# Kernel tuning notes

Hardware: AMD Instinct MI355X
Metric: run time of the kernel (lower is better)

The kernel has to match this reference:

```python
import jax, jax.numpy as jnp
from jax import lax
import numpy as np

BETA, TAU, NUM_ITER = 0.33, 1.0, 5
DN = ('NCDHW', 'OIDHW', 'NCDHW')


def _base_kernels():
    # 3x3x3 neighborhood-counting kernels from the torch module
    K_N6 = np.zeros((3, 3, 3), np.float32)
    for c in [(1, 1, 0), (1, 1, 2), (1, 0, 1), (1, 2, 1), (0, 1, 1), (2, 1, 1)]:
        K_N6[c] = 1.0
    K_N26 = np.ones((3, 3, 3), np.float32); K_N26[1, 1, 1] = 0.0
    K_N18 = K_N26.copy()
    for c in [(0, 0, 0), (0, 0, 2), (0, 2, 0), (0, 2, 2), (2, 0, 0), (2, 0, 2), (2, 2, 0), (2, 2, 2)]:
        K_N18[c] = 0.0
    K_B26 = np.zeros((3, 3, 3), np.float32)
    K_B26[0, 0, 0] = 1.0
    for c in [(0, 0, 1), (0, 1, 0), (0, 1, 1), (1, 0, 0), (1, 0, 1), (1, 1, 0)]:
        K_B26[c] = -1.0
    K_A6 = np.zeros((3, 3, 3), np.float32)
    K_A6[0, 1, 1] = -1.0
    for c in [(0, 0, 1), (0, 1, 0), (0, 1, 2), (0, 2, 1)]:
        K_A6[c] = 1.0
    return K_N6, K_N26, K_N18, K_B26, K_A6


def _stacked_weight():
    # Fuse all 17 simple-check convolutions into one conv over a 3-channel input
    # channel 0: img, channel 1: 1-img, channel 2: 2*img-1
    K_N6, K_N26, K_N18, K_B26, K_A6 = _base_kernels()
    b26 = [K_B26] + [np.flip(K_B26, ax) for ax in [(0,), (1,), (2,), (0, 1), (0, 2), (1, 2), (0, 1, 2)]]
    fA = np.flip(K_A6, 0)
    a6 = [K_A6, np.rot90(K_A6, axes=(0, 1)), np.rot90(K_A6, axes=(0, 2)),
          fA, np.rot90(fA, axes=(0, 1)), np.rot90(fA, axes=(0, 2))]
    rows = []
    def put(k, ch):
        w = np.zeros((3, 3, 3, 3), np.float32)
        w[ch] = k
        rows.append(w)
    put(K_N6, 1)   # counts bg 6-neighbors (applied to 1-img)
    put(K_N26, 0)  # counts fg 26-neighbors
    put(K_N18, 0)  # counts fg 18-neighbors
    for k in b26:
        put(k, 2)  # 8 B26-cell detectors on 2*img-1
    for k in a6:
        put(k, 2)  # 6 A6-cell detectors on 2*img-1
    return jnp.asarray(np.stack(rows)), jnp.asarray(K_N26).reshape(1, 1, 3, 3, 3)


W_SIMPLE, W_N26 = _stacked_weight()


def _clip01(x):  # F.hardtanh(x, 0, 1)
    return jnp.clip(x, 0.0, 1.0)


def _endpoint_check(img):
    p = jnp.pad(img, ((0, 0), (0, 0), (1, 1), (1, 1), (1, 1)))
    n26 = lax.conv_general_dilated(p, W_N26, (1, 1, 1), 'VALID', dimension_numbers=DN)
    return _clip01(2.0 - n26)  # endpoint iff <=1 fg 26-neighbor


def _simple_check(img):
    p = jnp.pad(img, ((0, 0), (0, 0), (1, 1), (1, 1), (1, 1)))
    x3 = jnp.concatenate([p, 1.0 - p, 2.0 * p - 1.0], axis=1)
    f = lax.conv_general_dilated(x3, W_SIMPLE, (2, 2, 2), 'VALID', dimension_numbers=DN)
    n6, n26, n18 = f[:, 0:1], f[:, 1:2], f[:, 2:3]
    num_b26 = jax.nn.relu(f[:, 3:11] - 6.0).sum(axis=1, keepdims=True)
    num_a6 = jax.nn.relu(f[:, 11:17] - 4.0).sum(axis=1, keepdims=True)
    cond1 = _clip01(n6) * _clip01(2.0 - n6)                              # exactly one bg 6-neighbor
    cond2 = _clip01(n26) * _clip01(2.0 - n26)                            # exactly one fg 26-neighbor
    cond3 = _clip01(n18) * _clip01(2.0 - n18) * _clip01(1.0 - num_b26)   # one 18-neighbor, no B26 cell
    cond4 = _clip01(n6 - 1.0) * _clip01(1.0 - num_a6) * _clip01(1.0 - num_b26)  # >=2 bg 6-nb, no A6/B26 cell
    return _clip01(cond1 + cond2 + cond3 + cond4)


def _forward(img):
    # _prepare_input: zero-pad each spatial dim by 1
    img = jnp.pad(img, ((0, 0), (0, 0), (1, 1), (1, 1), (1, 1)))
    # _stochastic_discretization (reparametrization + straight-through)
    alpha = (img + 1e-8) / (1.0 - img + 1e-8)
    u = jax.random.uniform(jax.random.key(42), img.shape, img.dtype, 1e-8, 1.0 - 1e-8)
    noise = jnp.log(u) - jnp.log1p(-u)
    soft = jax.nn.sigmoid((jnp.log(alpha) + noise * BETA) / TAU)
    img = lax.stop_gradient((soft > 0.5).astype(soft.dtype) - soft) + soft
    offsets = [(0, 0, 0), (1, 0, 0), (0, 1, 0), (1, 1, 0), (0, 0, 1), (1, 0, 1), (0, 1, 1), (1, 1, 1)]
    for _ in range(NUM_ITER):
        is_end = _endpoint_check(img)
        for xo, yo, zo in offsets:
            is_simple = _simple_check(img[:, :, xo:, yo:, zo:])
            sl = (slice(None), slice(None), slice(xo, None, 2), slice(yo, None, 2), slice(zo, None, 2))
            del_cand = is_simple * (1.0 - is_end[sl])
            img = img.at[sl].set(jnp.minimum(img[sl], 1.0 - del_cand))
    # _prepare_output: strip padding
    return img[:, :, 1:-1, 1:-1, 1:-1]


def setup_inputs():
    key = jax.random.key(0)
    img = jax.random.uniform(key, (2, 1, 160, 160, 160), jnp.float32)  # probabilities in [0,1)
    return {"img": img}


def reference(img):
    return _forward(img)
```

## Files before the change

kernel.cpp:

```cpp
#include <hip/hip_runtime.h>
#include <stdint.h>

#pragma clang fp contract(off)

#define PDIM 162
#define NW   (2*PDIM*PDIM*3)
#define NWH  (NW/2)
#define OD   160

#define PZ 97
#define LADDR(lz,ly) ((lz)*PZ + (ly)*3)

__device__ __forceinline__ uint32_t rotl32(uint32_t x, uint32_t r) {
  return (x << r) | (x >> (32u - r));
}

__device__ __forceinline__ uint32_t threefry_bits(uint32_t idx) {
  const uint32_t ks0 = 0u, ks1 = 42u, ks2 = 0x1BD11BDAu ^ 0u ^ 42u;
  uint32_t x0 = 0u + ks0;
  uint32_t x1 = idx + ks1;
#define TFR(r) { x0 += x1; x1 = rotl32(x1, (r)); x1 ^= x0; }
  TFR(13u) TFR(15u) TFR(26u) TFR(6u)
  x0 += ks1; x1 += ks2 + 1u;
  TFR(17u) TFR(29u) TFR(16u) TFR(24u)
  x0 += ks2; x1 += ks0 + 2u;
  TFR(13u) TFR(15u) TFR(26u) TFR(6u)
  x0 += ks0; x1 += ks1 + 3u;
  TFR(17u) TFR(29u) TFR(16u) TFR(24u)
  x0 += ks1; x1 += ks2 + 4u;
  TFR(13u) TFR(15u) TFR(26u) TFR(6u)
  x0 += ks2; x1 += ks0 + 5u;
#undef TFR
  return x0 ^ x1;
}

__device__ __forceinline__ float xla_logf(float xin) {
  uint32_t bits = __float_as_uint(xin);
  float e = (float)((int)(bits >> 23) - 126);
  float x = __uint_as_float((bits & 0x007fffffu) | 0x3f000000u);
  const float SQRTHF = 0.707106781186547524f;
  bool lt = (x < SQRTHF);
  float tmp = lt ? x : 0.0f;
  e = e - (lt ? 1.0f : 0.0f);
  x = x - 1.0f;
  x = x + tmp;
  float z = x * x;
  float y = 7.0376836292e-2f;
  y = fmaf(y, x, -1.1514610310e-1f);
  y = fmaf(y, x,  1.1676998740e-1f);
  y = fmaf(y, x, -1.2420140846e-1f);
  y = fmaf(y, x,  1.4249322787e-1f);
  y = fmaf(y, x, -1.6668057665e-1f);
  y = fmaf(y, x,  2.0000714765e-1f);
  y = fmaf(y, x, -2.4999993993e-1f);
  y = fmaf(y, x,  3.3333331174e-1f);
  y = y * x;
  y = y * z;
  y = fmaf(e, -2.12194440e-4f, y);
  y = fmaf(-0.5f, z, y);
  x = x + y;
  x = fmaf(e, 0.693359375f, x);
  return x;
}

__device__ __forceinline__ float xla_log1pf(float x) {
  float for_large = xla_logf(x + 1.0f);
  float for_small = fmaf(-0.5f, x, 1.0f) * x;
  return (fabsf(x) < 1e-4f) ? for_small : for_large;
}

__device__ __forceinline__ bool bin_pred(const float* __restrict__ in, uint32_t w,
                                         uint32_t lane) {
  uint32_t row = w / 3u, wx = w - row * 3u;
  uint32_t n  = row / (uint32_t)(PDIM * PDIM);
  uint32_t rr = row - n * (uint32_t)(PDIM * PDIM);
  uint32_t z  = rr / (uint32_t)PDIM;
  uint32_t y  = rr - z * (uint32_t)PDIM;
  uint32_t x  = wx * 64u + lane;
  if ((z - 1u) >= 160u || (y - 1u) >= 160u || (x - 1u) >= 160u) return false;
  float v = in[((n * 160u + (z - 1u)) * 160u + (y - 1u)) * 160u + (x - 1u)];
  uint32_t i = row * 162u + x;
  uint32_t b = threefry_bits(i);
  float f  = __uint_as_float((b >> 9) | 0x3f800000u) - 1.0f;
  float uu = fmaxf(1e-8f, f + 1e-8f);
  float la = xla_logf((v + 1e-8f) / ((1.0f - v) + 1e-8f));
  float noise = xla_logf(uu) - xla_log1pf(-uu);
  float zs = la + noise * 0.33f;
  return (zs > 1.1920928955078125e-7f);
}

__global__ __launch_bounds__(256) void k_binarize(const float* __restrict__ in,
                                                  uint64_t* __restrict__ bits) {
  uint32_t t = blockIdx.x * 256u + threadIdx.x;
  uint32_t w0 = t >> 6, lane = t & 63u;
  if (w0 >= (uint32_t)NWH) return;
  uint32_t w1 = w0 + (uint32_t)NWH;
  bool p0 = bin_pred(in, w0, lane);
  bool p1 = bin_pred(in, w1, lane);
  uint64_t m0 = __ballot(p0);
  uint64_t m1 = __ballot(p1);
  if (lane == 0) { bits[w0] = m0; bits[w1] = m1; }
}

#define NB(dz,dy,dx) ((dx)==-1 ? Lb[(dz)+1][(dy)+1] : ((dx)==1 ? Rb[(dz)+1][(dy)+1] : Vv[(dz)+1][(dy)+1]))

#define GATHER_W(SRC, lz, ly, w) \
  _Pragma("unroll") \
  for (int dz = 0; dz < 3; ++dz) \
    _Pragma("unroll") \
    for (int dy = 0; dy < 3; ++dy) { \
      int rb = LADDR((lz) + dz - 1, (ly) + dy - 1); \
      uint64_t r0 = SRC[rb], r1 = SRC[rb + 1], r2 = SRC[rb + 2]; \
      uint64_t b = ((w) == 0) ? r0 : (((w) == 1) ? r1 : r2); \
      uint64_t a = ((w) == 0) ? 0ull : (((w) == 1) ? r0 : r1); \
      uint64_t d = ((w) == 0) ? r1 : (((w) == 1) ? r2 : 0ull); \
      Vv[dz][dy] = b; \
      Lb[dz][dy] = (b << 1) | (a >> 63); \
      Rb[dz][dy] = (b >> 1) | (d << 63); \
    }

__global__ __launch_bounds__(1024) void k_iter(const uint64_t* __restrict__ bin,
                                               uint64_t* __restrict__ bout,
                                               float4* __restrict__ outf,
                                               int zero_pads) {
  __shared__ uint64_t Bt[32 * PZ];
  __shared__ uint64_t Ge[32 * PZ];
  const int tid = threadIdx.x;
  const int bid = blockIdx.x;
  const int n  = bid / 100;
  const int rm = bid - n * 100;
  const int tz = rm / 10, ty = rm - tz * 10;
  const int gz0 = 1 + 16 * tz, gy0 = 1 + 16 * ty;

  if (zero_pads && bid == 0) {
    for (int j = tid; j < 1288; j += 1024) {
      int nn, z, y;
      if (j < 648) { nn = j / 324; int r = j - nn * 324;
                     z = (r >= 162) ? 161 : 0; y = (r >= 162) ? r - 162 : r; }
      else { int j2 = j - 648; nn = j2 / 320; int r = j2 - nn * 320;
             y = (r >= 160) ? 161 : 0; z = 1 + ((r >= 160) ? r - 160 : r); }
      uint64_t* p = bout + (((nn * 162 + z) * 162) + y) * 3;
      p[0] = 0; p[1] = 0; p[2] = 0;
    }
  }

  for (int ti = tid; ti < 32 * 32 * 3; ti += 1024) {
    int w = ti % 3, r = ti / 3, ly = r % 32, lz = r / 32;
    int z = gz0 - 8 + lz, y = gy0 - 8 + ly;
    uint64_t v = 0;
    if ((unsigned)z < 162u && (unsigned)y < 162u)
      v = bin[((n * 162 + z) * 162 + y) * 3 + w];
    Bt[LADDR(lz, ly) + w] = v;
  }
  __syncthreads();

  for (int ti = tid; ti < 30 * 30 * 3; ti += 1024) {
    int w = ti % 3, r = ti / 3, iy = r % 30, iz = r / 30;
    int lz = 1 + iz, ly = 1 + iy;
    int base = LADDR(lz, ly) + w;
    uint64_t res = 0;
    if (Bt[base] != 0ull) {
      uint64_t Vv[3][3], Lb[3][3], Rb[3][3];
      GATHER_W(Bt, lz, ly, w)
      uint64_t s = 0, c = 0;
#define ACC(bb) { uint64_t _b = (bb); c |= s & _b; s |= _b; }
#pragma unroll
      for (int dz = -1; dz <= 1; ++dz)
#pragma unroll
        for (int dy = -1; dy <= 1; ++dy) {
          ACC(NB(dz,dy,-1)); ACC(NB(dz,dy,1));
          if (dz != 0 || dy != 0) ACC(NB(dz,dy,0));
        }
#undef ACC
      res = c;
    }
    Ge[base] = res;
  }
  __syncthreads();

  const int PLZ[8] = {1,0,1,0,1,0,1,0};
  const int PLY[8] = {1,1,0,0,1,1,0,0};
  for (int k = 0; k < 8; ++k) {
    const int h = 7 - k, cnt1 = 8 + h;
    const uint64_t xmask = (k < 4) ? 0x5555555555555555ull : 0xAAAAAAAAAAAAAAAAull;
    int s0 = 8 - h;
    const int slz = s0 + ((s0 ^ PLZ[k]) & 1);
    const int sly = s0 + ((s0 ^ PLY[k]) & 1);
    for (int ti = tid; ti < cnt1 * cnt1 * 3; ti += 1024) {
      int w = ti % 3, r = ti / 3, iy = r % cnt1, iz = r / cnt1;
      int lz = slz + 2 * iz, ly = sly + 2 * iy;
      int base = LADDR(lz, ly) + w;
      uint64_t center = Bt[base];
      uint64_t active = center & xmask & Ge[base];
      if (active == 0ull) continue;
      uint64_t Vv[3][3], Lb[3][3], Rb[3][3];
      GATHER_W(Bt, lz, ly, w)

      uint64_t on = 0, tw = 0, fo = 0;
#define C6ADD(b) { uint64_t _u = on & (b); on ^= (b); uint64_t _v = tw & _u; tw ^= _u; fo |= _v; }
      C6ADD(NB(-1,0,0)) C6ADD(NB(1,0,0)) C6ADD(NB(0,-1,0))
      C6ADD(NB(0,1,0))  C6ADD(NB(0,0,-1)) C6ADD(NB(0,0,1))
#undef C6ADD
      uint64_t c6eq5 = fo & on & ~tw;
      uint64_t c6le4 = ~(fo & (on | tw));

      uint64_t s = 0, c2 = 0;
#define CS(b) { uint64_t _b = (b); c2 |= s & _b; s |= _b; }
      CS(NB(-1,0,0)) CS(NB(1,0,0)) CS(NB(0,-1,0)) CS(NB(0,1,0)) CS(NB(0,0,-1)) CS(NB(0,0,1))
      CS(NB(-1,-1,0)) CS(NB(-1,1,0)) CS(NB(-1,0,-1)) CS(NB(-1,0,1))
      CS(NB(1,-1,0))  CS(NB(1,1,0))  CS(NB(1,0,-1))  CS(NB(1,0,1))
      CS(NB(0,-1,-1)) CS(NB(0,-1,1)) CS(NB(0,1,-1))  CS(NB(0,1,1))
      uint64_t e18 = s & ~c2;
      CS(NB(-1,-1,-1)) CS(NB(-1,-1,1)) CS(NB(-1,1,-1)) CS(NB(-1,1,1))
      CS(NB(1,-1,-1))  CS(NB(1,-1,1))  CS(NB(1,1,-1))  CS(NB(1,1,1))
      uint64_t e26 = s & ~c2;
#undef CS

      uint64_t badB = 0;
#pragma unroll
      for (int sz = -1; sz <= 1; sz += 2)
#pragma unroll
        for (int sy = -1; sy <= 1; sy += 2)
#pragma unroll
          for (int sx = -1; sx <= 1; sx += 2) {
            uint64_t oct = NB(sz,0,0) | NB(0,sy,0) | NB(0,0,sx)
                         | NB(sz,sy,0) | NB(sz,0,sx) | NB(0,sy,sx);
            badB |= NB(sz,sy,sx) & ~oct;
          }
      uint64_t b0ok = ~badB;

      uint64_t badA = 0;
      badA |= ~NB(-1,0,0) & NB(-1,-1,0) & NB(-1,1,0) & NB(-1,0,-1) & NB(-1,0,1);
      badA |= ~NB( 1,0,0) & NB( 1,-1,0) & NB( 1,1,0) & NB( 1,0,-1) & NB( 1,0,1);
      badA |= ~NB(0,-1,0) & NB(-1,-1,0) & NB(1,-1,0) & NB(0,-1,-1) & NB(0,-1,1);
      badA |= ~NB(0, 1,0) & NB(-1, 1,0) & NB(1, 1,0) & NB(0, 1,-1) & NB(0, 1,1);
      badA |= ~NB(0,0,-1) & NB(-1,0,-1) & NB(1,0,-1) & NB(0,-1,-1) & NB(0,1,-1);
      badA |= ~NB(0,0, 1) & NB(-1,0, 1) & NB(1,0, 1) & NB(0,-1, 1) & NB(0,1, 1);
      uint64_t a0ok = ~badA;

      uint64_t simple = c6eq5 | e26 | (e18 & b0ok) | (c6le4 & a0ok & b0ok);
      uint64_t del = simple & active;
      if (del) Bt[base] = center & ~del;
    }
    __syncthreads();
  }

  if (outf) {
    for (int ti = tid; ti < 16 * 16 * 40; ti += 1024) {
      int g = ti % 40, r = ti / 40, iy = r % 16, iz = r / 16;
      int base = LADDR(8 + iz, 8 + iy);
      int bi = 1 + 4 * g;
      int wx = bi >> 6, sft = bi & 63;
      uint64_t v = Bt[base + wx] >> sft;
      if (sft > 60) v |= Bt[base + wx + 1] << (64 - sft);
      outf[((n * 160 + (gz0 + iz - 1)) * 160 + (gy0 + iy - 1)) * 40 + g] =
          make_float4((float)(v & 1u), (float)((v >> 1) & 1u),
                      (float)((v >> 2) & 1u), (float)((v >> 3) & 1u));
    }
  } else {
    for (int ti = tid; ti < 16 * 16 * 3; ti += 1024) {
      int w = ti % 3, r = ti / 3, iy = r % 16, iz = r / 16;
      bout[((n * 162 + gz0 + iz) * 162 + (gy0 + iy)) * 3 + w] =
          Bt[LADDR(8 + iz, 8 + iy) + w];
    }
  }
}

extern "C" void kernel_launch(void* const* d_in, const int* in_sizes, int n_in,
                              void* d_out, int out_size, void* d_ws, size_t ws_size,
                              hipStream_t stream) {
  const float* in = (const float*)d_in[0];
  float4* out = (float4*)d_out;
  uint64_t* A = (uint64_t*)d_ws;
  uint64_t* B = A + NW;

  k_binarize<<<dim3((NWH * 64 + 255) / 256), dim3(256), 0, stream>>>(in, A);
  k_iter<<<dim3(200), dim3(1024), 0, stream>>>(A, B, nullptr, 1);
  k_iter<<<dim3(200), dim3(1024), 0, stream>>>(B, A, nullptr, 0);
  k_iter<<<dim3(200), dim3(1024), 0, stream>>>(A, B, nullptr, 0);
  k_iter<<<dim3(200), dim3(1024), 0, stream>>>(B, A, nullptr, 0);
  k_iter<<<dim3(200), dim3(1024), 0, stream>>>(A, nullptr, out, 0);
}
```

Before: 228.7 us.

## Process all three x-words per thread and skip B/A checks when unneeded

Each thread now handles a whole (z,y) row of three 64-bit words instead of one word. It loads the 3x3x3 neighbourhood words once and reuses them across the three words, which cuts redundant shared-memory loads and index arithmetic in both the endpoint pass and the eight deletion sub-iterations. The B26/A6 octant checks are evaluated only when some active bits are not already decided by the cheap c6eq5/e26 tests, and the k loop is unrolled. The cost is fewer threads doing useful work per sub-iteration, since tile counts drop threefold against 1024 threads, plus higher register pressure from the 27-word cache.

```diff
diff --git a/kernel.cpp b/kernel.cpp
--- a/kernel.cpp
+++ b/kernel.cpp
@@ -104,19 +104,26 @@
 
 #define NB(dz,dy,dx) ((dx)==-1 ? Lb[(dz)+1][(dy)+1] : ((dx)==1 ? Rb[(dz)+1][(dy)+1] : Vv[(dz)+1][(dy)+1]))
 
-#define GATHER_W(SRC, lz, ly, w) \
+#define EXPAND_W(w_) \
+  _Pragma("unroll") \
+  for (int dz = 0; dz < 3; ++dz) \
+    _Pragma("unroll") \
+    for (int dy = 0; dy < 3; ++dy) { \
+      uint64_t b = R[dz][dy][w_]; \
+      uint64_t a = ((w_) > 0) ? R[dz][dy][(w_)-1] : 0ull; \
+      uint64_t d = ((w_) < 2) ? R[dz][dy][(w_)+1] : 0ull; \
+      Vv[dz][dy] = b; \
+      Lb[dz][dy] = (b << 1) | (a >> 63); \
+      Rb[dz][dy] = (b >> 1) | (d << 63); \
+    }
+
+#define LOAD_R(SRC, lz, ly) \
   _Pragma("unroll") \
   for (int dz = 0; dz < 3; ++dz) \
     _Pragma("unroll") \
     for (int dy = 0; dy < 3; ++dy) { \
       int rb = LADDR((lz) + dz - 1, (ly) + dy - 1); \
-      uint64_t r0 = SRC[rb], r1 = SRC[rb + 1], r2 = SRC[rb + 2]; \
-      uint64_t b = ((w) == 0) ? r0 : (((w) == 1) ? r1 : r2); \
-      uint64_t a = ((w) == 0) ? 0ull : (((w) == 1) ? r0 : r1); \
-      uint64_t d = ((w) == 0) ? r1 : (((w) == 1) ? r2 : 0ull); \
-      Vv[dz][dy] = b; \
-      Lb[dz][dy] = (b << 1) | (a >> 63); \
-      Rb[dz][dy] = (b >> 1) | (d << 63); \
+      R[dz][dy][0] = SRC[rb]; R[dz][dy][1] = SRC[rb + 1]; R[dz][dy][2] = SRC[rb + 2]; \
     }
 
 __global__ __launch_bounds__(1024) void k_iter(const uint64_t* __restrict__ bin,
@@ -154,14 +161,18 @@
   }
   __syncthreads();
 
-  for (int ti = tid; ti < 30 * 30 * 3; ti += 1024) {
-    int w = ti % 3, r = ti / 3, iy = r % 30, iz = r / 30;
+  for (int ti = tid; ti < 30 * 30; ti += 1024) {
+    int iy = ti % 30, iz = ti / 30;
     int lz = 1 + iz, ly = 1 + iy;
-    int base = LADDR(lz, ly) + w;
-    uint64_t res = 0;
-    if (Bt[base] != 0ull) {
+    int base = LADDR(lz, ly);
+    uint64_t c0 = Bt[base], c1 = Bt[base + 1], c2c = Bt[base + 2];
+    if ((c0 | c1 | c2c) == 0ull) { Ge[base] = 0; Ge[base+1] = 0; Ge[base+2] = 0; continue; }
+    uint64_t R[3][3][3];
+    LOAD_R(Bt, lz, ly)
+#pragma unroll
+    for (int w = 0; w < 3; ++w) {
       uint64_t Vv[3][3], Lb[3][3], Rb[3][3];
-      GATHER_W(Bt, lz, ly, w)
+      EXPAND_W(w)
       uint64_t s = 0, c = 0;
 #define ACC(bb) { uint64_t _b = (bb); c |= s & _b; s |= _b; }
 #pragma unroll
@@ -172,75 +183,88 @@
           if (dz != 0 || dy != 0) ACC(NB(dz,dy,0));
         }
 #undef ACC
-      res = c;
-    }
-    Ge[base] = res;
+      Ge[base + w] = c;
+    }
   }
   __syncthreads();
 
   const int PLZ[8] = {1,0,1,0,1,0,1,0};
   const int PLY[8] = {1,1,0,0,1,1,0,0};
+#pragma unroll
   for (int k = 0; k < 8; ++k) {
     const int h = 7 - k, cnt1 = 8 + h;
     const uint64_t xmask = (k < 4) ? 0x5555555555555555ull : 0xAAAAAAAAAAAAAAAAull;
-    int s0 = 8 - h;
+    const int s0 = 8 - h;
     const int slz = s0 + ((s0 ^ PLZ[k]) & 1);
     const int sly = s0 + ((s0 ^ PLY[k]) & 1);
-    for (int ti = tid; ti < cnt1 * cnt1 * 3; ti += 1024) {
-      int w = ti % 3, r = ti / 3, iy = r % cnt1, iz = r / cnt1;
+    for (int ti = tid; ti < cnt1 * cnt1; ti += 1024) {
+      int iy = ti % cnt1, iz = ti / cnt1;
       int lz = slz + 2 * iz, ly = sly + 2 * iy;
-      int base = LADDR(lz, ly) + w;
-      uint64_t center = Bt[base];
-      uint64_t active = center & xmask & Ge[base];
-      if (active == 0ull) continue;
-      uint64_t Vv[3][3], Lb[3][3], Rb[3][3];
-      GATHER_W(Bt, lz, ly, w)
-
-      uint64_t on = 0, tw = 0, fo = 0;
+      int base = LADDR(lz, ly);
+      uint64_t ctr[3], act[3];
+#pragma unroll
+      for (int w = 0; w < 3; ++w) {
+        ctr[w] = Bt[base + w];
+        act[w] = ctr[w] & xmask & Ge[base + w];
+      }
+      if ((act[0] | act[1] | act[2]) == 0ull) continue;
+      uint64_t R[3][3][3];
+      LOAD_R(Bt, lz, ly)
+#pragma unroll
+      for (int w = 0; w < 3; ++w) {
+        if (act[w] == 0ull) continue;
+        uint64_t Vv[3][3], Lb[3][3], Rb[3][3];
+        EXPAND_W(w)
+
+        uint64_t on = 0, tw = 0, fo = 0;
 #define C6ADD(b) { uint64_t _u = on & (b); on ^= (b); uint64_t _v = tw & _u; tw ^= _u; fo |= _v; }
-      C6ADD(NB(-1,0,0)) C6ADD(NB(1,0,0)) C6ADD(NB(0,-1,0))
-      C6ADD(NB(0,1,0))  C6ADD(NB(0,0,-1)) C6ADD(NB(0,0,1))
+        C6ADD(NB(-1,0,0)) C6ADD(NB(1,0,0)) C6ADD(NB(0,-1,0))
+        C6ADD(NB(0,1,0))  C6ADD(NB(0,0,-1)) C6ADD(NB(0,0,1))
 #undef C6ADD
-      uint64_t c6eq5 = fo & on & ~tw;
-      uint64_t c6le4 = ~(fo & (on | tw));
-
-      uint64_t s = 0, c2 = 0;
+        uint64_t c6eq5 = fo & on & ~tw;
+        uint64_t c6le4 = ~(fo & (on | tw));
+
+        uint64_t s = 0, c2 = 0;
 #define CS(b) { uint64_t _b = (b); c2 |= s & _b; s |= _b; }
-      CS(NB(-1,0,0)) CS(NB(1,0,0)) CS(NB(0,-1,0)) CS(NB(0,1,0)) CS(NB(0,0,-1)) CS(NB(0,0,1))
-      CS(NB(-1,-1,0)) CS(NB(-1,1,0)) CS(NB(-1,0,-1)) CS(NB(-1,0,1))
-      CS(NB(1,-1,0))  CS(NB(1,1,0))  CS(NB(1,0,-1))  CS(NB(1,0,1))
-      CS(NB(0,-1,-1)) CS(NB(0,-1,1)) CS(NB(0,1,-1))  CS(NB(0,1,1))
-      uint64_t e18 = s & ~c2;
-      CS(NB(-1,-1,-1)) CS(NB(-1,-1,1)) CS(NB(-1,1,-1)) CS(NB(-1,1,1))
-      CS(NB(1,-1,-1))  CS(NB(1,-1,1))  CS(NB(1,1,-1))  CS(NB(1,1,1))
-      uint64_t e26 = s & ~c2;
+        CS(NB(-1,0,0)) CS(NB(1,0,0)) CS(NB(0,-1,0)) CS(NB(0,1,0)) CS(NB(0,0,-1)) CS(NB(0,0,1))
+        CS(NB(-1,-1,0)) CS(NB(-1,1,0)) CS(NB(-1,0,-1)) CS(NB(-1,0,1))
+        CS(NB(1,-1,0))  CS(NB(1,1,0))  CS(NB(1,0,-1))  CS(NB(1,0,1))
+        CS(NB(0,-1,-1)) CS(NB(0,-1,1)) CS(NB(0,1,-1))  CS(NB(0,1,1))
+        uint64_t e18 = s & ~c2;
+        CS(NB(-1,-1,-1)) CS(NB(-1,-1,1)) CS(NB(-1,1,-1)) CS(NB(-1,1,1))
+        CS(NB(1,-1,-1))  CS(NB(1,-1,1))  CS(NB(1,1,-1))  CS(NB(1,1,1))
+        uint64_t e26 = s & ~c2;
 #undef CS
 
-      uint64_t badB = 0;
-#pragma unroll
-      for (int sz = -1; sz <= 1; sz += 2)
-#pragma unroll
-        for (int sy = -1; sy <= 1; sy += 2)
-#pragma unroll
-          for (int sx = -1; sx <= 1; sx += 2) {
-            uint64_t oct = NB(sz,0,0) | NB(0,sy,0) | NB(0,0,sx)
-                         | NB(sz,sy,0) | NB(sz,0,sx) | NB(0,sy,sx);
-            badB |= NB(sz,sy,sx) & ~oct;
-          }
-      uint64_t b0ok = ~badB;
-
-      uint64_t badA = 0;
-      badA |= ~NB(-1,0,0) & NB(-1,-1,0) & NB(-1,1,0) & NB(-1,0,-1) & NB(-1,0,1);
-      badA |= ~NB( 1,0,0) & NB( 1,-1,0) & NB( 1,1,0) & NB( 1,0,-1) & NB( 1,0,1);
-      badA |= ~NB(0,-1,0) & NB(-1,-1,0) & NB(1,-1,0) & NB(0,-1,-1) & NB(0,-1,1);
-      badA |= ~NB(0, 1,0) & NB(-1, 1,0) & NB(1, 1,0) & NB(0, 1,-1) & NB(0, 1,1);
-      badA |= ~NB(0,0,-1) & NB(-1,0,-1) & NB(1,0,-1) & NB(0,-1,-1) & NB(0,1,-1);
-      badA |= ~NB(0,0, 1) & NB(-1,0, 1) & NB(1,0, 1) & NB(0,-1, 1) & NB(0,1, 1);
-      uint64_t a0ok = ~badA;
-
-      uint64_t simple = c6eq5 | e26 | (e18 & b0ok) | (c6le4 & a0ok & b0ok);
-      uint64_t del = simple & active;
-      if (del) Bt[base] = center & ~del;
+        uint64_t del = (c6eq5 | e26) & act[w];
+        uint64_t need = act[w] & ~del & (e18 | c6le4);
+        if (need != 0ull) {
+          uint64_t badB = 0;
+#pragma unroll
+          for (int sz = -1; sz <= 1; sz += 2)
+#pragma unroll
+            for (int sy = -1; sy <= 1; sy += 2)
+#pragma unroll
+              for (int sx = -1; sx <= 1; sx += 2) {
+                uint64_t oct = NB(sz,0,0) | NB(0,sy,0) | NB(0,0,sx)
+                             | NB(sz,sy,0) | NB(sz,0,sx) | NB(0,sy,sx);
+                badB |= NB(sz,sy,sx) & ~oct;
+              }
+          uint64_t b0ok = ~badB;
+
+          uint64_t badA = 0;
+          badA |= ~NB(-1,0,0) & NB(-1,-1,0) & NB(-1,1,0) & NB(-1,0,-1) & NB(-1,0,1);
+          badA |= ~NB( 1,0,0) & NB( 1,-1,0) & NB( 1,1,0) & NB( 1,0,-1) & NB( 1,0,1);
+          badA |= ~NB(0,-1,0) & NB(-1,-1,0) & NB(1,-1,0) & NB(0,-1,-1) & NB(0,-1,1);
+          badA |= ~NB(0, 1,0) & NB(-1, 1,0) & NB(1, 1,0) & NB(0, 1,-1) & NB(0, 1,1);
+          badA |= ~NB(0,0,-1) & NB(-1,0,-1) & NB(1,0,-1) & NB(0,-1,-1) & NB(0,1,-1);
+          badA |= ~NB(0,0, 1) & NB(-1,0, 1) & NB(1,0, 1) & NB(0,-1, 1) & NB(0,1, 1);
+          uint64_t a0ok = ~badA;
+
+          del |= ((e18 & b0ok) | (c6le4 & a0ok & b0ok)) & act[w];
+        }
+        if (del) Bt[base + w] = ctr[w] & ~del;
+      }
     }
     __syncthreads();
   }
```

Measured after the change: 253.5 us. +10.8%, slower.

## Compute endpoint mask lazily per candidate and skip B/A checks when unneeded

Applied to the files above, without the earlier changes.

Removes the separate endpoint-precompute pass over the whole 30x30 tile. It keeps an unmodified copy of the initial tile in shared memory (B0) and computes the endpoint mask on demand, only for words with candidate voxels in each subiteration. It also skips the expensive B26/A6 cell checks when the cheaper conditions already decide deletion, and unrolls the 8-offset loop. In exchange, endpoint counting can be redone per subiteration for overlapping words, the kernel does an extra gather from B0, and shared memory now holds a full second tile copy.

```diff
diff --git a/kernel.cpp b/kernel.cpp
--- a/kernel.cpp
+++ b/kernel.cpp
@@ -124,7 +124,7 @@
                                                float4* __restrict__ outf,
                                                int zero_pads) {
   __shared__ uint64_t Bt[32 * PZ];
-  __shared__ uint64_t Ge[32 * PZ];
+  __shared__ uint64_t B0[32 * PZ];
   const int tid = threadIdx.x;
   const int bid = blockIdx.x;
   const int n  = bid / 100;
@@ -151,39 +151,17 @@
     if ((unsigned)z < 162u && (unsigned)y < 162u)
       v = bin[((n * 162 + z) * 162 + y) * 3 + w];
     Bt[LADDR(lz, ly) + w] = v;
-  }
-  __syncthreads();
-
-  for (int ti = tid; ti < 30 * 30 * 3; ti += 1024) {
-    int w = ti % 3, r = ti / 3, iy = r % 30, iz = r / 30;
-    int lz = 1 + iz, ly = 1 + iy;
-    int base = LADDR(lz, ly) + w;
-    uint64_t res = 0;
-    if (Bt[base] != 0ull) {
-      uint64_t Vv[3][3], Lb[3][3], Rb[3][3];
-      GATHER_W(Bt, lz, ly, w)
-      uint64_t s = 0, c = 0;
-#define ACC(bb) { uint64_t _b = (bb); c |= s & _b; s |= _b; }
-#pragma unroll
-      for (int dz = -1; dz <= 1; ++dz)
-#pragma unroll
-        for (int dy = -1; dy <= 1; ++dy) {
-          ACC(NB(dz,dy,-1)); ACC(NB(dz,dy,1));
-          if (dz != 0 || dy != 0) ACC(NB(dz,dy,0));
-        }
-#undef ACC
-      res = c;
-    }
-    Ge[base] = res;
+    B0[LADDR(lz, ly) + w] = v;
   }
   __syncthreads();
 
   const int PLZ[8] = {1,0,1,0,1,0,1,0};
   const int PLY[8] = {1,1,0,0,1,1,0,0};
+#pragma unroll
   for (int k = 0; k < 8; ++k) {
     const int h = 7 - k, cnt1 = 8 + h;
     const uint64_t xmask = (k < 4) ? 0x5555555555555555ull : 0xAAAAAAAAAAAAAAAAull;
-    int s0 = 8 - h;
+    const int s0 = 8 - h;
     const int slz = s0 + ((s0 ^ PLZ[k]) & 1);
     const int sly = s0 + ((s0 ^ PLY[k]) & 1);
     for (int ti = tid; ti < cnt1 * cnt1 * 3; ti += 1024) {
@@ -191,10 +169,25 @@
       int lz = slz + 2 * iz, ly = sly + 2 * iy;
       int base = LADDR(lz, ly) + w;
       uint64_t center = Bt[base];
-      uint64_t active = center & xmask & Ge[base];
-      if (active == 0ull) continue;
+      uint64_t pre = center & xmask;
+      if (pre == 0ull) continue;
+
       uint64_t Vv[3][3], Lb[3][3], Rb[3][3];
-      GATHER_W(Bt, lz, ly, w)
+      if (k == 0) { GATHER_W(Bt, lz, ly, w) }
+      else        { GATHER_W(B0, lz, ly, w) }
+      uint64_t s = 0, c2 = 0;
+#define CS(b) { uint64_t _b = (b); c2 |= s & _b; s |= _b; }
+#pragma unroll
+      for (int dz = -1; dz <= 1; ++dz)
+#pragma unroll
+        for (int dy = -1; dy <= 1; ++dy) {
+          CS(NB(dz,dy,-1)); CS(NB(dz,dy,1));
+          if (dz != 0 || dy != 0) CS(NB(dz,dy,0));
+        }
+      uint64_t act = pre & c2;
+      if (act == 0ull) continue;
+
+      if (k != 0) { GATHER_W(Bt, lz, ly, w) }
 
       uint64_t on = 0, tw = 0, fo = 0;
 #define C6ADD(b) { uint64_t _u = on & (b); on ^= (b); uint64_t _v = tw & _u; tw ^= _u; fo |= _v; }
@@ -204,8 +197,7 @@
       uint64_t c6eq5 = fo & on & ~tw;
       uint64_t c6le4 = ~(fo & (on | tw));
 
-      uint64_t s = 0, c2 = 0;
-#define CS(b) { uint64_t _b = (b); c2 |= s & _b; s |= _b; }
+      s = 0; c2 = 0;
       CS(NB(-1,0,0)) CS(NB(1,0,0)) CS(NB(0,-1,0)) CS(NB(0,1,0)) CS(NB(0,0,-1)) CS(NB(0,0,1))
       CS(NB(-1,-1,0)) CS(NB(-1,1,0)) CS(NB(-1,0,-1)) CS(NB(-1,0,1))
       CS(NB(1,-1,0))  CS(NB(1,1,0))  CS(NB(1,0,-1))  CS(NB(1,0,1))
@@ -216,30 +208,33 @@
       uint64_t e26 = s & ~c2;
 #undef CS
 
-      uint64_t badB = 0;
-#pragma unroll
-      for (int sz = -1; sz <= 1; sz += 2)
-#pragma unroll
-        for (int sy = -1; sy <= 1; sy += 2)
-#pragma unroll
-          for (int sx = -1; sx <= 1; sx += 2) {
-            uint64_t oct = NB(sz,0,0) | NB(0,sy,0) | NB(0,0,sx)
-                         | NB(sz,sy,0) | NB(sz,0,sx) | NB(0,sy,sx);
-            badB |= NB(sz,sy,sx) & ~oct;
-          }
-      uint64_t b0ok = ~badB;
-
-      uint64_t badA = 0;
-      badA |= ~NB(-1,0,0) & NB(-1,-1,0) & NB(-1,1,0) & NB(-1,0,-1) & NB(-1,0,1);
-      badA |= ~NB( 1,0,0) & NB( 1,-1,0) & NB( 1,1,0) & NB( 1,0,-1) & NB( 1,0,1);
-      badA |= ~NB(0,-1,0) & NB(-1,-1,0) & NB(1,-1,0) & NB(0,-1,-1) & NB(0,-1,1);
-      badA |= ~NB(0, 1,0) & NB(-1, 1,0) & NB(1, 1,0) & NB(0, 1,-1) & NB(0, 1,1);
-      badA |= ~NB(0,0,-1) & NB(-1,0,-1) & NB(1,0,-1) & NB(0,-1,-1) & NB(0,1,-1);
-      badA |= ~NB(0,0, 1) & NB(-1,0, 1) & NB(1,0, 1) & NB(0,-1, 1) & NB(0,1, 1);
-      uint64_t a0ok = ~badA;
-
-      uint64_t simple = c6eq5 | e26 | (e18 & b0ok) | (c6le4 & a0ok & b0ok);
-      uint64_t del = simple & active;
+      uint64_t del = (c6eq5 | e26) & act;
+      uint64_t need = act & ~del & (e18 | c6le4);
+      if (need != 0ull) {
+        uint64_t badB = 0;
+#pragma unroll
+        for (int sz = -1; sz <= 1; sz += 2)
+#pragma unroll
+          for (int sy = -1; sy <= 1; sy += 2)
+#pragma unroll
+            for (int sx = -1; sx <= 1; sx += 2) {
+              uint64_t oct = NB(sz,0,0) | NB(0,sy,0) | NB(0,0,sx)
+                           | NB(sz,sy,0) | NB(sz,0,sx) | NB(0,sy,sx);
+              badB |= NB(sz,sy,sx) & ~oct;
+            }
+        uint64_t b0ok = ~badB;
+
+        uint64_t badA = 0;
+        badA |= ~NB(-1,0,0) & NB(-1,-1,0) & NB(-1,1,0) & NB(-1,0,-1) & NB(-1,0,1);
+        badA |= ~NB( 1,0,0) & NB( 1,-1,0) & NB( 1,1,0) & NB( 1,0,-1) & NB( 1,0,1);
+        badA |= ~NB(0,-1,0) & NB(-1,-1,0) & NB(1,-1,0) & NB(0,-1,-1) & NB(0,-1,1);
+        badA |= ~NB(0, 1,0) & NB(-1, 1,0) & NB(1, 1,0) & NB(0, 1,-1) & NB(0, 1,1);
+        badA |= ~NB(0,0,-1) & NB(-1,0,-1) & NB(1,0,-1) & NB(0,-1,-1) & NB(0,1,-1);
+        badA |= ~NB(0,0, 1) & NB(-1,0, 1) & NB(1,0, 1) & NB(0,-1, 1) & NB(0,1, 1);
+        uint64_t a0ok = ~badA;
+
+        del |= ((e18 & b0ok) | (c6le4 & a0ok & b0ok)) & act;
+      }
       if (del) Bt[base] = center & ~del;
     }
     __syncthreads();
```

After: 236.1 us. +3.2%, slower.
